# Kernel optimization log

Measured on AMD Instinct MI355X. Metric: run time of the kernel, lower is better.

## Reference

```python
import jax, jax.numpy as jnp
import numpy as np

B, NC, F, V, D = 16384, 13, 26, 100000, 16
H1, H2 = 400, 400
DNN_IN = NC + F * D  # 13 + 416 = 429


def setup_inputs() -> dict:
    key = jax.random.key(0)
    ks = jax.random.split(key, 12)
    s = 0.02
    return {
        "continuous": jax.random.normal(ks[0], (B, NC), jnp.float32),
        "cat_idx": jax.random.randint(ks[1], (B, F), 0, V),
        "W_cont": jax.random.normal(ks[2], (NC, 1), jnp.float32) * s,
        "b_cont": jnp.zeros((1,), jnp.float32),
        "emb_first": jax.random.normal(ks[3], (F, V), jnp.float32) * s,
        "emb": jax.random.normal(ks[4], (F, V, D), jnp.float32) * s,
        "W1": jax.random.normal(ks[5], (DNN_IN, H1), jnp.float32) * s,
        "b1": jnp.zeros((H1,), jnp.float32),
        "W2": jax.random.normal(ks[6], (H1, H2), jnp.float32) * s,
        "b2": jnp.zeros((H2,), jnp.float32),
        "W_out": jax.random.normal(ks[7], (H2 + 1, 1), jnp.float32) * s,
        "b_out": jnp.zeros((1,), jnp.float32),
    }


def reference(continuous, cat_idx, W_cont, b_cont, emb_first, emb, W1, b1, W2, b2, W_out, b_out):
    f_ids = jnp.arange(F)  # column ids
    # FM first-order: continuous linear + per-column 1-dim embedding gather, summed over columns
    fm1_cat = emb_first[f_ids[None, :], cat_idx]          # [B, F]
    fm1 = continuous @ W_cont + b_cont + jnp.sum(fm1_cat, axis=1, keepdims=True)  # [B, 1]
    # FM second-order: per-column D-dim embedding gather
    E = emb[f_ids[None, :], cat_idx]                      # [B, F, D]
    sum_emb = jnp.sum(E, axis=1)                          # [B, D]
    fm2 = 0.5 * jnp.sum(sum_emb * sum_emb - jnp.sum(E * E, axis=1), axis=1, keepdims=True)  # [B, 1]
    fm_out = fm1 + fm2
    # DNN on [continuous | flattened embeddings]; Dropout(0.0) is identity
    dnn_in = jnp.concatenate([continuous, E.reshape(E.shape[0], -1)], axis=1)  # [B, 429]
    h = jax.nn.relu(dnn_in @ W1 + b1)
    h = jax.nn.relu(h @ W2 + b2)
    fusion = jnp.concatenate([fm_out, h], axis=1)         # [B, H2+1]
    return fusion @ W_out + b_out                          # [B, 1]
```

## Files before the change

### kernel.cpp

```cpp
#include <hip/hip_runtime.h>
#include <hip/hip_bf16.h>
#include <stdint.h>

#define NB    16384
#define NCONT 13
#define NF    26
#define NV    100000
#define ND    16
#define NH    400
#define K1    448
#define KP1   456
#define K2    416
#define KP2   424
#define NPAD  448
#define NJ    7
#define ROWS  32

typedef __attribute__((ext_vector_type(8))) __bf16 bf16x8;
typedef __attribute__((ext_vector_type(8))) short short8;
typedef __attribute__((ext_vector_type(4))) float f32x4;

__device__ __forceinline__ short f2bf(float x) {
  union { float f; uint32_t u; } c; c.f = x;
  uint32_t r = (c.u + 0x7FFFu + ((c.u >> 16) & 1u)) >> 16;
  return (short)(uint16_t)r;
}

__global__ __launch_bounds__(256)
void prep_k(const float* __restrict__ W1, const float* __restrict__ W2,
            short* __restrict__ W1T, short* __restrict__ W2T) {
  int t = blockIdx.x * 256 + threadIdx.x;
  if (t < NPAD * K1) {
    int n = t / K1, k = t - n * K1;
    float v = 0.f;
    if (n < NH) {
      if (k < 416)       v = W1[(size_t)(13 + k) * NH + n];
      else if (k < 429)  v = W1[(size_t)(k - 416) * NH + n];
    }
    W1T[t] = f2bf(v);
  } else {
    int u = t - NPAD * K1;
    int n = u / K2, k = u - n * K2;
    float v = (n < NH && k < NH) ? W2[(size_t)k * NH + n] : 0.f;
    W2T[u] = f2bf(v);
  }
}

__global__ __launch_bounds__(256)
void gather_k(const float* __restrict__ cont, const int* __restrict__ cat,
              const float* __restrict__ Wc, const float* __restrict__ bc,
              const float* __restrict__ emb1, const float* __restrict__ emb,
              const float* __restrict__ Wout, const float* __restrict__ bout,
              short* __restrict__ dnn, float* __restrict__ out) {
  const int t = blockIdx.x * 256 + threadIdx.x;
  const int b = t >> 3;
  const int q = t & 7;
  float se[16];
#pragma unroll
  for (int d = 0; d < 16; d++) se[d] = 0.f;
  float sumsq = 0.f, fm1 = 0.f;
  short* drow = dnn + (size_t)b * K1;

#pragma unroll
  for (int fi = 0; fi < 4; fi++) {
    const int f = q + 8 * fi;
    if (fi == 3 && q >= 2) break;
    int idx = cat[(size_t)b * NF + f];
    const float4* ep = (const float4*)(emb + ((size_t)f * NV + idx) * ND);
    float4 e0 = ep[0], e1 = ep[1], e2 = ep[2], e3 = ep[3];
    fm1 += emb1[(size_t)f * NV + idx];
    se[0] += e0.x; se[1] += e0.y; se[2] += e0.z; se[3] += e0.w;
    se[4] += e1.x; se[5] += e1.y; se[6] += e1.z; se[7] += e1.w;
    se[8] += e2.x; se[9] += e2.y; se[10] += e2.z; se[11] += e2.w;
    se[12] += e3.x; se[13] += e3.y; se[14] += e3.z; se[15] += e3.w;
    sumsq += e0.x*e0.x + e0.y*e0.y + e0.z*e0.z + e0.w*e0.w
           + e1.x*e1.x + e1.y*e1.y + e1.z*e1.z + e1.w*e1.w
           + e2.x*e2.x + e2.y*e2.y + e2.z*e2.z + e2.w*e2.w
           + e3.x*e3.x + e3.y*e3.y + e3.z*e3.z + e3.w*e3.w;
    short8 p0, p1;
    p0[0]=f2bf(e0.x); p0[1]=f2bf(e0.y); p0[2]=f2bf(e0.z); p0[3]=f2bf(e0.w);
    p0[4]=f2bf(e1.x); p0[5]=f2bf(e1.y); p0[6]=f2bf(e1.z); p0[7]=f2bf(e1.w);
    p1[0]=f2bf(e2.x); p1[1]=f2bf(e2.y); p1[2]=f2bf(e2.z); p1[3]=f2bf(e2.w);
    p1[4]=f2bf(e3.x); p1[5]=f2bf(e3.y); p1[6]=f2bf(e3.z); p1[7]=f2bf(e3.w);
    *(short8*)(drow + f * 16)     = p0;
    *(short8*)(drow + f * 16 + 8) = p1;
  }
#pragma unroll
  for (int d = 0; d < 16; d++) {
    se[d] += __shfl_xor(se[d], 1, 64);
    se[d] += __shfl_xor(se[d], 2, 64);
    se[d] += __shfl_xor(se[d], 4, 64);
  }
  sumsq += __shfl_xor(sumsq, 1, 64);
  sumsq += __shfl_xor(sumsq, 2, 64);
  sumsq += __shfl_xor(sumsq, 4, 64);
  fm1   += __shfl_xor(fm1, 1, 64);
  fm1   += __shfl_xor(fm1, 2, 64);
  fm1   += __shfl_xor(fm1, 4, 64);

  if (q == 0) {
    float s2 = 0.f;
#pragma unroll
    for (int d = 0; d < 16; d++) s2 += se[d] * se[d];
    float fm2 = 0.5f * (s2 - sumsq);
    float fmc = bc[0];
    short tail[32];
#pragma unroll
    for (int i = 0; i < NCONT; i++) {
      float c = cont[(size_t)b * NCONT + i];
      fmc += c * Wc[i];
      tail[i] = f2bf(c);
    }
#pragma unroll
    for (int i = NCONT; i < 32; i++) tail[i] = 0;
#pragma unroll
    for (int v = 0; v < 4; v++) {
      short8 tv;
#pragma unroll
      for (int e = 0; e < 8; e++) tv[e] = tail[v * 8 + e];
      *(short8*)(drow + 416 + v * 8) = tv;
    }
    out[b] = (fm1 + fmc + fm2) * Wout[0] + bout[0];
  }
}

template <int K, int KP>
__device__ __forceinline__ void layer(const short* __restrict__ WT, const short* lds,
                                      int wave, int lrow, int kq, f32x4 acc[2][NJ]) {
  const short* wp[NJ];
#pragma unroll
  for (int j = 0; j < NJ; j++)
    wp[j] = WT + (size_t)((wave + 4 * j) * 16 + lrow) * K + kq;
  bf16x8 wf[2][NJ], af[2][2];
#pragma unroll
  for (int j = 0; j < NJ; j++) wf[0][j] = *(const bf16x8*)(wp[j]);
#pragma unroll
  for (int i = 0; i < 2; i++) af[0][i] = *(const bf16x8*)(lds + (i * 16 + lrow) * KP + kq);
#pragma unroll
  for (int ks = 0; ks < K / 32; ks++) {
    const int cur = ks & 1, nxt = cur ^ 1;
    if (ks + 1 < K / 32) {
#pragma unroll
      for (int j = 0; j < NJ; j++) wf[nxt][j] = *(const bf16x8*)(wp[j] + (ks + 1) * 32);
#pragma unroll
      for (int i = 0; i < 2; i++)
        af[nxt][i] = *(const bf16x8*)(lds + (i * 16 + lrow) * KP + (ks + 1) * 32 + kq);
    }
#pragma unroll
    for (int i = 0; i < 2; i++)
#pragma unroll
      for (int j = 0; j < NJ; j++)
        acc[i][j] = __builtin_amdgcn_mfma_f32_16x16x32_bf16(af[cur][i], wf[cur][j], acc[i][j], 0, 0, 0);
  }
}

__global__ __launch_bounds__(256, 2)
void dnn_k(const short* __restrict__ dnn,
           const short* __restrict__ W1T, const float* __restrict__ b1,
           const short* __restrict__ W2T, const float* __restrict__ b2,
           const float* __restrict__ Wout, float* __restrict__ out) {
  __shared__ short lA[ROWS * KP1];
  __shared__ short lH[ROWS * KP2];
  const int tid = threadIdx.x;
  const int bm = blockIdx.x * ROWS;

  {
    const int r = tid >> 3, s = (tid & 7) * 56;
    const short* g = dnn + (size_t)(bm + r) * K1 + s;
    short* l = &lA[r * KP1 + s];
#pragma unroll
    for (int c = 0; c < 7; c++)
      *(short8*)(l + c * 8) = *(const short8*)(g + c * 8);
  }
  __syncthreads();

  const int lane = tid & 63;
  const int wave = tid >> 6;
  const int lrow = lane & 15;
  const int quad = lane >> 4;
  const int kq   = quad * 8;
  f32x4 acc[2][NJ];

#pragma unroll
  for (int i = 0; i < 2; i++)
#pragma unroll
    for (int j = 0; j < NJ; j++)
#pragma unroll
      for (int r = 0; r < 4; r++) acc[i][j][r] = 0.f;
  layer<K1, KP1>(W1T, lA, wave, lrow, kq, acc);

#pragma unroll
  for (int j = 0; j < NJ; j++) {
    int col = (wave + 4 * j) * 16 + lrow;
    if (col < K2) {
      float bias = (col < NH) ? b1[col] : 0.f;
#pragma unroll
      for (int i = 0; i < 2; i++)
#pragma unroll
        for (int r = 0; r < 4; r++) {
          int row = i * 16 + quad * 4 + r;
          float v = (col < NH) ? fmaxf(acc[i][j][r] + bias, 0.f) : 0.f;
          lH[row * KP2 + col] = f2bf(v);
        }
    }
  }
  __syncthreads();

#pragma unroll
  for (int i = 0; i < 2; i++)
#pragma unroll
    for (int j = 0; j < NJ; j++)
#pragma unroll
      for (int r = 0; r < 4; r++) acc[i][j][r] = 0.f;
  layer<K2, KP2>(W2T, lH, wave, lrow, kq, acc);

  {
    float bw[NJ], wo[NJ];
#pragma unroll
    for (int j = 0; j < NJ; j++) {
      int col = (wave + 4 * j) * 16 + lrow;
      bw[j] = (col < NH) ? b2[col] : 0.f;
      wo[j] = (col < NH) ? Wout[1 + col] : 0.f;
    }
#pragma unroll
    for (int i = 0; i < 2; i++) {
#pragma unroll
      for (int r = 0; r < 4; r++) {
        float s = 0.f;
#pragma unroll
        for (int j = 0; j < NJ; j++)
          s += fmaxf(acc[i][j][r] + bw[j], 0.f) * wo[j];
        s += __shfl_xor(s, 1, 64);
        s += __shfl_xor(s, 2, 64);
        s += __shfl_xor(s, 4, 64);
        s += __shfl_xor(s, 8, 64);
        if (lrow == 0) atomicAdd(&out[bm + i * 16 + quad * 4 + r], s);
      }
    }
  }
}

extern "C" void kernel_launch(void* const* d_in, const int* in_sizes, int n_in,
                              void* d_out, int out_size, void* d_ws, size_t ws_size,
                              hipStream_t stream) {
  const float* cont   = (const float*)d_in[0];
  const int*   cat    = (const int*)d_in[1];
  const float* W_cont = (const float*)d_in[2];
  const float* b_cont = (const float*)d_in[3];
  const float* emb1   = (const float*)d_in[4];
  const float* emb    = (const float*)d_in[5];
  const float* W1     = (const float*)d_in[6];
  const float* b1     = (const float*)d_in[7];
  const float* W2     = (const float*)d_in[8];
  const float* b2     = (const float*)d_in[9];
  const float* W_out  = (const float*)d_in[10];
  const float* b_out  = (const float*)d_in[11];
  float* out = (float*)d_out;

  char* ws = (char*)d_ws;
  size_t off = 0;
  short* dnn = (short*)(ws + off); off += (size_t)NB * K1 * 2;
  short* W1T = (short*)(ws + off); off += (size_t)NPAD * K1 * 2;
  short* W2T = (short*)(ws + off); off += (size_t)NPAD * K2 * 2;
  (void)ws_size; (void)in_sizes; (void)n_in; (void)out_size;

  prep_k<<<dim3((NPAD * K1 + NPAD * K2) / 256), dim3(256), 0, stream>>>(W1, W2, W1T, W2T);
  gather_k<<<dim3(NB * 8 / 256), dim3(256), 0, stream>>>(cont, cat, W_cont, b_cont,
                                                         emb1, emb, W_out, b_out, dnn, out);
  dnn_k<<<dim3(NB / ROWS), dim3(256), 0, stream>>>(dnn, W1T, b1, W2T, b2, W_out, out);
}
```

Baseline: 285.5 us.

## Fuse embedding gather into MLP kernel with 64-row tiles and unpadded weights

Merges the gather/FM kernel into the MLP kernel, so the bf16 DNN input is built directly in LDS and never goes through a global workspace. The row tile doubles to 64 per block, sharing each weight fetch across more rows. Weight padding from 448 to 400 columns is dropped, so only wave 0 handles the seventh column tile. The output is now written once per row after an LDS reduction instead of atomics. The costs are occupancy limited to one block per SM due to larger LDS and register use, and gather latency no longer overlapping with a separate kernel.

```diff
diff --git a/kernel.cpp b/kernel.cpp
--- a/kernel.cpp
+++ b/kernel.cpp
@@ -12,9 +12,7 @@
 #define KP1   456
 #define K2    416
 #define KP2   424
-#define NPAD  448
-#define NJ    7
-#define ROWS  32
+#define ROWS  64
 
 typedef __attribute__((ext_vector_type(8))) __bf16 bf16x8;
 typedef __attribute__((ext_vector_type(8))) short short8;
@@ -30,147 +28,138 @@
 void prep_k(const float* __restrict__ W1, const float* __restrict__ W2,
             short* __restrict__ W1T, short* __restrict__ W2T) {
   int t = blockIdx.x * 256 + threadIdx.x;
-  if (t < NPAD * K1) {
+  if (t < NH * K1) {
     int n = t / K1, k = t - n * K1;
     float v = 0.f;
-    if (n < NH) {
-      if (k < 416)       v = W1[(size_t)(13 + k) * NH + n];
-      else if (k < 429)  v = W1[(size_t)(k - 416) * NH + n];
-    }
+    if (k < 416)       v = W1[(size_t)(13 + k) * NH + n];
+    else if (k < 429)  v = W1[(size_t)(k - 416) * NH + n];
     W1T[t] = f2bf(v);
   } else {
-    int u = t - NPAD * K1;
+    int u = t - NH * K1;
     int n = u / K2, k = u - n * K2;
-    float v = (n < NH && k < NH) ? W2[(size_t)k * NH + n] : 0.f;
+    float v = (k < NH) ? W2[(size_t)k * NH + n] : 0.f;
     W2T[u] = f2bf(v);
-  }
-}
-
-__global__ __launch_bounds__(256)
-void gather_k(const float* __restrict__ cont, const int* __restrict__ cat,
-              const float* __restrict__ Wc, const float* __restrict__ bc,
-              const float* __restrict__ emb1, const float* __restrict__ emb,
-              const float* __restrict__ Wout, const float* __restrict__ bout,
-              short* __restrict__ dnn, float* __restrict__ out) {
-  const int t = blockIdx.x * 256 + threadIdx.x;
-  const int b = t >> 3;
-  const int q = t & 7;
-  float se[16];
-#pragma unroll
-  for (int d = 0; d < 16; d++) se[d] = 0.f;
-  float sumsq = 0.f, fm1 = 0.f;
-  short* drow = dnn + (size_t)b * K1;
-
-#pragma unroll
-  for (int fi = 0; fi < 4; fi++) {
-    const int f = q + 8 * fi;
-    if (fi == 3 && q >= 2) break;
-    int idx = cat[(size_t)b * NF + f];
-    const float4* ep = (const float4*)(emb + ((size_t)f * NV + idx) * ND);
-    float4 e0 = ep[0], e1 = ep[1], e2 = ep[2], e3 = ep[3];
-    fm1 += emb1[(size_t)f * NV + idx];
-    se[0] += e0.x; se[1] += e0.y; se[2] += e0.z; se[3] += e0.w;
-    se[4] += e1.x; se[5] += e1.y; se[6] += e1.z; se[7] += e1.w;
-    se[8] += e2.x; se[9] += e2.y; se[10] += e2.z; se[11] += e2.w;
-    se[12] += e3.x; se[13] += e3.y; se[14] += e3.z; se[15] += e3.w;
-    sumsq += e0.x*e0.x + e0.y*e0.y + e0.z*e0.z + e0.w*e0.w
-           + e1.x*e1.x + e1.y*e1.y + e1.z*e1.z + e1.w*e1.w
-           + e2.x*e2.x + e2.y*e2.y + e2.z*e2.z + e2.w*e2.w
-           + e3.x*e3.x + e3.y*e3.y + e3.z*e3.z + e3.w*e3.w;
-    short8 p0, p1;
-    p0[0]=f2bf(e0.x); p0[1]=f2bf(e0.y); p0[2]=f2bf(e0.z); p0[3]=f2bf(e0.w);
-    p0[4]=f2bf(e1.x); p0[5]=f2bf(e1.y); p0[6]=f2bf(e1.z); p0[7]=f2bf(e1.w);
-    p1[0]=f2bf(e2.x); p1[1]=f2bf(e2.y); p1[2]=f2bf(e2.z); p1[3]=f2bf(e2.w);
-    p1[4]=f2bf(e3.x); p1[5]=f2bf(e3.y); p1[6]=f2bf(e3.z); p1[7]=f2bf(e3.w);
-    *(short8*)(drow + f * 16)     = p0;
-    *(short8*)(drow + f * 16 + 8) = p1;
-  }
-#pragma unroll
-  for (int d = 0; d < 16; d++) {
-    se[d] += __shfl_xor(se[d], 1, 64);
-    se[d] += __shfl_xor(se[d], 2, 64);
-    se[d] += __shfl_xor(se[d], 4, 64);
-  }
-  sumsq += __shfl_xor(sumsq, 1, 64);
-  sumsq += __shfl_xor(sumsq, 2, 64);
-  sumsq += __shfl_xor(sumsq, 4, 64);
-  fm1   += __shfl_xor(fm1, 1, 64);
-  fm1   += __shfl_xor(fm1, 2, 64);
-  fm1   += __shfl_xor(fm1, 4, 64);
-
-  if (q == 0) {
-    float s2 = 0.f;
-#pragma unroll
-    for (int d = 0; d < 16; d++) s2 += se[d] * se[d];
-    float fm2 = 0.5f * (s2 - sumsq);
-    float fmc = bc[0];
-    short tail[32];
-#pragma unroll
-    for (int i = 0; i < NCONT; i++) {
-      float c = cont[(size_t)b * NCONT + i];
-      fmc += c * Wc[i];
-      tail[i] = f2bf(c);
-    }
-#pragma unroll
-    for (int i = NCONT; i < 32; i++) tail[i] = 0;
-#pragma unroll
-    for (int v = 0; v < 4; v++) {
-      short8 tv;
-#pragma unroll
-      for (int e = 0; e < 8; e++) tv[e] = tail[v * 8 + e];
-      *(short8*)(drow + 416 + v * 8) = tv;
-    }
-    out[b] = (fm1 + fmc + fm2) * Wout[0] + bout[0];
   }
 }
 
 template <int K, int KP>
 __device__ __forceinline__ void layer(const short* __restrict__ WT, const short* lds,
-                                      int wave, int lrow, int kq, f32x4 acc[2][NJ]) {
-  const short* wp[NJ];
-#pragma unroll
-  for (int j = 0; j < NJ; j++)
-    wp[j] = WT + (size_t)((wave + 4 * j) * 16 + lrow) * K + kq;
-  bf16x8 wf[2][NJ], af[2][2];
-#pragma unroll
-  for (int j = 0; j < NJ; j++) wf[0][j] = *(const bf16x8*)(wp[j]);
-#pragma unroll
-  for (int i = 0; i < 2; i++) af[0][i] = *(const bf16x8*)(lds + (i * 16 + lrow) * KP + kq);
+                                      int wave, bool w0, int lrow, int kq,
+                                      f32x4 acc[4][7]) {
+  const short* wb = WT + (size_t)(wave * 16 + lrow) * K + kq;
+  bf16x8 wf[2][7], af[2][4];
+#pragma unroll
+  for (int j = 0; j < 7; j++)
+    if (j < 6 || w0) wf[0][j] = *(const bf16x8*)(wb + (size_t)j * 64 * K);
+#pragma unroll
+  for (int i = 0; i < 4; i++)
+    af[0][i] = *(const bf16x8*)(lds + (i * 16 + lrow) * KP + kq);
 #pragma unroll
   for (int ks = 0; ks < K / 32; ks++) {
     const int cur = ks & 1, nxt = cur ^ 1;
     if (ks + 1 < K / 32) {
 #pragma unroll
-      for (int j = 0; j < NJ; j++) wf[nxt][j] = *(const bf16x8*)(wp[j] + (ks + 1) * 32);
-#pragma unroll
-      for (int i = 0; i < 2; i++)
+      for (int j = 0; j < 7; j++)
+        if (j < 6 || w0)
+          wf[nxt][j] = *(const bf16x8*)(wb + (size_t)j * 64 * K + (ks + 1) * 32);
+#pragma unroll
+      for (int i = 0; i < 4; i++)
         af[nxt][i] = *(const bf16x8*)(lds + (i * 16 + lrow) * KP + (ks + 1) * 32 + kq);
     }
 #pragma unroll
-    for (int i = 0; i < 2; i++)
-#pragma unroll
-      for (int j = 0; j < NJ; j++)
-        acc[i][j] = __builtin_amdgcn_mfma_f32_16x16x32_bf16(af[cur][i], wf[cur][j], acc[i][j], 0, 0, 0);
-  }
-}
-
-__global__ __launch_bounds__(256, 2)
-void dnn_k(const short* __restrict__ dnn,
-           const short* __restrict__ W1T, const float* __restrict__ b1,
-           const short* __restrict__ W2T, const float* __restrict__ b2,
-           const float* __restrict__ Wout, float* __restrict__ out) {
-  __shared__ short lA[ROWS * KP1];
-  __shared__ short lH[ROWS * KP2];
+    for (int i = 0; i < 4; i++)
+#pragma unroll
+      for (int j = 0; j < 7; j++)
+        if (j < 6 || w0)
+          acc[i][j] = __builtin_amdgcn_mfma_f32_16x16x32_bf16(af[cur][i], wf[cur][j], acc[i][j], 0, 0, 0);
+  }
+}
+
+__global__ __launch_bounds__(256, 1)
+void fused_k(const float* __restrict__ cont, const int* __restrict__ cat,
+             const float* __restrict__ Wc, const float* __restrict__ bc,
+             const float* __restrict__ emb1, const float* __restrict__ emb,
+             const short* __restrict__ W1T, const float* __restrict__ b1,
+             const short* __restrict__ W2T, const float* __restrict__ b2,
+             const float* __restrict__ Wout, const float* __restrict__ bout,
+             float* __restrict__ out) {
+  __shared__ short buf[ROWS * KP1];
+  __shared__ float lP[4][ROWS];
+  __shared__ float lFM[ROWS];
+  short* lA = buf;
+  short* lH = buf;
   const int tid = threadIdx.x;
   const int bm = blockIdx.x * ROWS;
 
   {
-    const int r = tid >> 3, s = (tid & 7) * 56;
-    const short* g = dnn + (size_t)(bm + r) * K1 + s;
-    short* l = &lA[r * KP1 + s];
-#pragma unroll
-    for (int c = 0; c < 7; c++)
-      *(short8*)(l + c * 8) = *(const short8*)(g + c * 8);
+    const int q  = tid & 3;
+    const int rl = tid >> 2;
+    const int b  = bm + rl;
+    float se[16];
+#pragma unroll
+    for (int d = 0; d < 16; d++) se[d] = 0.f;
+    float sumsq = 0.f, fm1 = 0.f;
+    short* drow = lA + rl * KP1;
+
+#pragma unroll
+    for (int fi = 0; fi < 7; fi++) {
+      const int f = q + 4 * fi;
+      if (f < NF) {
+        int idx = cat[(size_t)b * NF + f];
+        const float4* ep = (const float4*)(emb + ((size_t)f * NV + idx) * ND);
+        float4 e0 = ep[0], e1 = ep[1], e2 = ep[2], e3 = ep[3];
+        fm1 += emb1[(size_t)f * NV + idx];
+        se[0] += e0.x; se[1] += e0.y; se[2] += e0.z; se[3] += e0.w;
+        se[4] += e1.x; se[5] += e1.y; se[6] += e1.z; se[7] += e1.w;
+        se[8] += e2.x; se[9] += e2.y; se[10] += e2.z; se[11] += e2.w;
+        se[12] += e3.x; se[13] += e3.y; se[14] += e3.z; se[15] += e3.w;
+        sumsq += e0.x*e0.x + e0.y*e0.y + e0.z*e0.z + e0.w*e0.w
+               + e1.x*e1.x + e1.y*e1.y + e1.z*e1.z + e1.w*e1.w
+               + e2.x*e2.x + e2.y*e2.y + e2.z*e2.z + e2.w*e2.w
+               + e3.x*e3.x + e3.y*e3.y + e3.z*e3.z + e3.w*e3.w;
+        short8 p0, p1;
+        p0[0]=f2bf(e0.x); p0[1]=f2bf(e0.y); p0[2]=f2bf(e0.z); p0[3]=f2bf(e0.w);
+        p0[4]=f2bf(e1.x); p0[5]=f2bf(e1.y); p0[6]=f2bf(e1.z); p0[7]=f2bf(e1.w);
+        p1[0]=f2bf(e2.x); p1[1]=f2bf(e2.y); p1[2]=f2bf(e2.z); p1[3]=f2bf(e2.w);
+        p1[4]=f2bf(e3.x); p1[5]=f2bf(e3.y); p1[6]=f2bf(e3.z); p1[7]=f2bf(e3.w);
+        *(short8*)(drow + f * 16)     = p0;
+        *(short8*)(drow + f * 16 + 8) = p1;
+      }
+    }
+#pragma unroll
+    for (int d = 0; d < 16; d++) {
+      se[d] += __shfl_xor(se[d], 1, 64);
+      se[d] += __shfl_xor(se[d], 2, 64);
+    }
+    sumsq += __shfl_xor(sumsq, 1, 64);
+    sumsq += __shfl_xor(sumsq, 2, 64);
+    fm1   += __shfl_xor(fm1, 1, 64);
+    fm1   += __shfl_xor(fm1, 2, 64);
+
+    if (q == 0) {
+      float s2 = 0.f;
+#pragma unroll
+      for (int d = 0; d < 16; d++) s2 += se[d] * se[d];
+      float fm2 = 0.5f * (s2 - sumsq);
+      float fmc = bc[0];
+      short tail[32];
+#pragma unroll
+      for (int i = 0; i < NCONT; i++) {
+        float c = cont[(size_t)b * NCONT + i];
+        fmc += c * Wc[i];
+        tail[i] = f2bf(c);
+      }
+#pragma unroll
+      for (int i = NCONT; i < 32; i++) tail[i] = 0;
+#pragma unroll
+      for (int v = 0; v < 4; v++) {
+        short8 tv;
+#pragma unroll
+        for (int e = 0; e < 8; e++) tv[e] = tail[v * 8 + e];
+        *(short8*)(drow + 416 + v * 8) = tv;
+      }
+      lFM[rl] = fm1 + fmc + fm2;
+    }
   }
   __syncthreads();
 
@@ -179,65 +168,79 @@
   const int lrow = lane & 15;
   const int quad = lane >> 4;
   const int kq   = quad * 8;
-  f32x4 acc[2][NJ];
-
-#pragma unroll
-  for (int i = 0; i < 2; i++)
-#pragma unroll
-    for (int j = 0; j < NJ; j++)
+  const bool w0  = (wave == 0);
+  f32x4 acc[4][7];
+
+#pragma unroll
+  for (int i = 0; i < 4; i++)
+#pragma unroll
+    for (int j = 0; j < 7; j++)
 #pragma unroll
       for (int r = 0; r < 4; r++) acc[i][j][r] = 0.f;
-  layer<K1, KP1>(W1T, lA, wave, lrow, kq, acc);
-
-#pragma unroll
-  for (int j = 0; j < NJ; j++) {
-    int col = (wave + 4 * j) * 16 + lrow;
-    if (col < K2) {
-      float bias = (col < NH) ? b1[col] : 0.f;
-#pragma unroll
-      for (int i = 0; i < 2; i++)
+  layer<K1, KP1>(W1T, lA, wave, w0, lrow, kq, acc);
+
+  __syncthreads();
+
+#pragma unroll
+  for (int j = 0; j < 7; j++) {
+    if (j < 6 || w0) {
+      int col = (wave + 4 * j) * 16 + lrow;
+      float bias = b1[col];
+#pragma unroll
+      for (int i = 0; i < 4; i++)
 #pragma unroll
         for (int r = 0; r < 4; r++) {
           int row = i * 16 + quad * 4 + r;
-          float v = (col < NH) ? fmaxf(acc[i][j][r] + bias, 0.f) : 0.f;
-          lH[row * KP2 + col] = f2bf(v);
+          lH[row * KP2 + col] = f2bf(fmaxf(acc[i][j][r] + bias, 0.f));
         }
     }
   }
-  __syncthreads();
-
-#pragma unroll
-  for (int i = 0; i < 2; i++)
-#pragma unroll
-    for (int j = 0; j < NJ; j++)
+  {
+    int row = tid >> 2, g = tid & 3;
+    *(uint2*)&lH[row * KP2 + 400 + g * 4] = make_uint2(0u, 0u);
+  }
+  __syncthreads();
+
+#pragma unroll
+  for (int i = 0; i < 4; i++)
+#pragma unroll
+    for (int j = 0; j < 7; j++)
 #pragma unroll
       for (int r = 0; r < 4; r++) acc[i][j][r] = 0.f;
-  layer<K2, KP2>(W2T, lH, wave, lrow, kq, acc);
+  layer<K2, KP2>(W2T, lH, wave, w0, lrow, kq, acc);
 
   {
-    float bw[NJ], wo[NJ];
-#pragma unroll
-    for (int j = 0; j < NJ; j++) {
-      int col = (wave + 4 * j) * 16 + lrow;
-      bw[j] = (col < NH) ? b2[col] : 0.f;
-      wo[j] = (col < NH) ? Wout[1 + col] : 0.f;
-    }
-#pragma unroll
-    for (int i = 0; i < 2; i++) {
+    float bw[7], wo[7];
+#pragma unroll
+    for (int j = 0; j < 7; j++) {
+      bw[j] = 0.f; wo[j] = 0.f;
+      if (j < 6 || w0) {
+        int col = (wave + 4 * j) * 16 + lrow;
+        bw[j] = b2[col];
+        wo[j] = Wout[1 + col];
+      }
+    }
+#pragma unroll
+    for (int i = 0; i < 4; i++) {
 #pragma unroll
       for (int r = 0; r < 4; r++) {
         float s = 0.f;
 #pragma unroll
-        for (int j = 0; j < NJ; j++)
-          s += fmaxf(acc[i][j][r] + bw[j], 0.f) * wo[j];
+        for (int j = 0; j < 7; j++)
+          if (j < 6 || w0) s += fmaxf(acc[i][j][r] + bw[j], 0.f) * wo[j];
         s += __shfl_xor(s, 1, 64);
         s += __shfl_xor(s, 2, 64);
         s += __shfl_xor(s, 4, 64);
         s += __shfl_xor(s, 8, 64);
-        if (lrow == 0) atomicAdd(&out[bm + i * 16 + quad * 4 + r], s);
-      }
-    }
-  }
+        if (lrow == 0) lP[wave][i * 16 + quad * 4 + r] = s;
+      }
+    }
+  }
+  __syncthreads();
+
+  if (tid < ROWS)
+    out[bm + tid] = lFM[tid] * Wout[0] + bout[0]
+                  + lP[0][tid] + lP[1][tid] + lP[2][tid] + lP[3][tid];
 }
 
 extern "C" void kernel_launch(void* const* d_in, const int* in_sizes, int n_in,
@@ -258,14 +261,12 @@
   float* out = (float*)d_out;
 
   char* ws = (char*)d_ws;
-  size_t off = 0;
-  short* dnn = (short*)(ws + off); off += (size_t)NB * K1 * 2;
-  short* W1T = (short*)(ws + off); off += (size_t)NPAD * K1 * 2;
-  short* W2T = (short*)(ws + off); off += (size_t)NPAD * K2 * 2;
+  short* W1T = (short*)ws;
+  short* W2T = (short*)(ws + (size_t)NH * K1 * 2);
   (void)ws_size; (void)in_sizes; (void)n_in; (void)out_size;
 
-  prep_k<<<dim3((NPAD * K1 + NPAD * K2) / 256), dim3(256), 0, stream>>>(W1, W2, W1T, W2T);
-  gather_k<<<dim3(NB * 8 / 256), dim3(256), 0, stream>>>(cont, cat, W_cont, b_cont,
-                                                         emb1, emb, W_out, b_out, dnn, out);
-  dnn_k<<<dim3(NB / ROWS), dim3(256), 0, stream>>>(dnn, W1T, b1, W2T, b2, W_out, out);
-}
+  prep_k<<<dim3((NH * K1 + NH * K2 + 255) / 256), dim3(256), 0, stream>>>(W1, W2, W1T, W2T);
+  fused_k<<<dim3(NB / ROWS), dim3(256), 0, stream>>>(cont, cat, W_cont, b_cont,
+                                                     emb1, emb, W1T, b1, W2T, b2,
+                                                     W_out, b_out, out);
+}
```

Result: faster. 271.0 us (-5.1%).
